# Optimization experiments

Measured on AMD Instinct MI355X. Metric: run time of the kernel, lower is better.

## Reference

```python
import jax, jax.numpy as jnp
import numpy as np

N = 100000
E = 1600000
DIMS = [64, 64, 64, 32]  # input -> hidden -> hidden -> num_classes
NEG_SLOPE = 0.01  # F.leaky_relu default


def setup_inputs() -> dict:
    key = jax.random.key(0)
    ks = jax.random.split(key, 8)
    inp = {
        "x": jax.random.normal(ks[0], (N, DIMS[0]), dtype=jnp.float32),
        "edge_index": jax.random.randint(ks[1], (2, E), 0, N, dtype=jnp.int64),
    }
    # GCNConv linear weights (glorot-ish scale) and biases
    for i in range(3):
        d_in, d_out = DIMS[i], DIMS[i + 1]
        scale = (2.0 / (d_in + d_out)) ** 0.5
        inp[f"W{i+1}"] = jax.random.normal(ks[2 + i], (d_in, d_out), dtype=jnp.float32) * scale
        inp[f"b{i+1}"] = jnp.zeros((d_out,), dtype=jnp.float32)
    return inp


def _gcn_conv(x, src, dst, norm, W, b):
    # x' = D^-1/2 (A+I) D^-1/2 (x W) + b
    h = x @ W                                   # [N, d_out]
    msg = h[src] * norm[:, None]                # gather + edge scaling  [E+N, d_out]
    out = jax.ops.segment_sum(msg, dst, num_segments=N)  # scatter-add
    return out + b


def reference(x, edge_index, W1, b1, W2, b2, W3, b3):
    loops = jnp.arange(N, dtype=edge_index.dtype)
    src = jnp.concatenate([edge_index[0], loops])  # add self-loops
    dst = jnp.concatenate([edge_index[1], loops])
    deg = jax.ops.segment_sum(jnp.ones_like(src, dtype=x.dtype), dst, num_segments=N)
    deg_isqrt = jax.lax.rsqrt(deg)              # deg >= 1 due to self-loops
    norm = deg_isqrt[src] * deg_isqrt[dst]      # [E+N]

    embeddings = []
    h = x
    for i, (W, b) in enumerate([(W1, b1), (W2, b2), (W3, b3)]):
        h = _gcn_conv(h, src, dst, norm, W, b)
        if i < 2:
            h = jnp.where(h >= 0, h, NEG_SLOPE * h)  # leaky_relu
        embeddings.append(h)
    return tuple(embeddings)
```

## Files before the change

### kernel.cpp

```cpp
#include <hip/hip_runtime.h>
#include <hip/hip_bf16.h>

typedef __hip_bfloat16 bf16;
typedef __attribute__((ext_vector_type(8))) short bf16x8;
typedef __attribute__((ext_vector_type(4))) short bf16x4;
typedef __attribute__((ext_vector_type(4))) float f32x4;

constexpr int BLK = 256;
constexpr int SCAN2_T = 512;
constexpr int NBLK = 400;

__device__ inline float s2f(short s) {
    union { unsigned u; float f; } z;
    z.u = ((unsigned)(unsigned short)s) << 16;
    return z.f;
}
__device__ inline short f2s(float f) {
    union { bf16 h; short s; } u;
    u.h = __float2bfloat16(f);
    return u.s;
}

__global__ void bucket_hist(const int* __restrict__ dst, int* __restrict__ blockhist,
                            int E, int EPB, int NB) {
    __shared__ int h[512];
    for (int i = threadIdx.x; i < NB; i += BLK) h[i] = 0;
    __syncthreads();
    int lo = blockIdx.x * EPB;
    int hi = min(E, lo + EPB);
    for (int t = lo + threadIdx.x; t < hi; t += BLK)
        atomicAdd(&h[dst[t] >> 8], 1);
    __syncthreads();
    for (int i = threadIdx.x; i < NB; i += BLK)
        blockhist[i * NBLK + blockIdx.x] = h[i];
}

__global__ void colscan_kernel(int* __restrict__ blockhist, int* __restrict__ btotal) {
    __shared__ int s[SCAN2_T];
    int b = blockIdx.x;
    int t = threadIdx.x;
    int v = (t < NBLK) ? blockhist[b * NBLK + t] : 0;
    s[t] = v;
    __syncthreads();
    for (int off = 1; off < SCAN2_T; off <<= 1) {
        int add = (t >= off) ? s[t - off] : 0;
        __syncthreads();
        s[t] += add;
        __syncthreads();
    }
    if (t < NBLK) blockhist[b * NBLK + t] = s[t] - v;
    if (t == SCAN2_T - 1) btotal[b] = s[SCAN2_T - 1];
}

__global__ void scan2_kernel(int* __restrict__ bsum, int nb) {
    __shared__ int s[SCAN2_T];
    int t = threadIdx.x;
    int v = (t < nb) ? bsum[t] : 0;
    s[t] = v;
    __syncthreads();
    for (int off = 1; off < SCAN2_T; off <<= 1) {
        int add = (t >= off) ? s[t - off] : 0;
        __syncthreads();
        s[t] += add;
        __syncthreads();
    }
    if (t < nb) bsum[t] = s[t] - v;
}

__global__ void bucket_scatter(const int* __restrict__ src, const int* __restrict__ dst,
                               const int* __restrict__ blockhist, const int* __restrict__ bbase,
                               int2* __restrict__ ssd, int E, int EPB, int NB) {
    __shared__ int h[512];
    for (int i = threadIdx.x; i < NB; i += BLK)
        h[i] = bbase[i] + blockhist[i * NBLK + blockIdx.x];
    __syncthreads();
    int lo = blockIdx.x * EPB;
    int hi = min(E, lo + EPB);
    for (int t = lo + threadIdx.x; t < hi; t += BLK) {
        int d = dst[t];
        int pos = atomicAdd(&h[d >> 8], 1);
        int2 e; e.x = src[t]; e.y = d;
        ssd[pos] = e;
    }
}

__global__ void bucket_csr(const int2* __restrict__ ssd, const int* __restrict__ bbase,
                           int* __restrict__ col, int* __restrict__ deg,
                           int* __restrict__ row_ptr, float* __restrict__ dinv,
                           int N, int E, int NB) {
    __shared__ int dloc[256];
    __shared__ int ss[256];
    __shared__ int cur[256];
    int b = blockIdx.x;
    int t = threadIdx.x;
    int lo = bbase[b];
    int hi = (b + 1 < NB) ? bbase[b + 1] : E;
    dloc[t] = 0;
    __syncthreads();
    for (int j = lo + t; j < hi; j += BLK)
        atomicAdd(&dloc[ssd[j].y & 255], 1);
    __syncthreads();
    int own = dloc[t];
    ss[t] = own;
    __syncthreads();
    for (int off = 1; off < 256; off <<= 1) {
        int add = (t >= off) ? ss[t - off] : 0;
        __syncthreads();
        ss[t] += add;
        __syncthreads();
    }
    int excl = ss[t] - own;
    cur[t] = lo + excl;
    int node = (b << 8) + t;
    if (node < N) {
        deg[node] = own;
        row_ptr[node] = lo + excl;
        dinv[node] = rsqrtf((float)own + 1.0f);
    }
    __syncthreads();
    for (int j = lo + t; j < hi; j += BLK) {
        int2 e = ssd[j];
        int p = atomicAdd(&cur[e.y & 255], 1);
        col[p] = e.x;
    }
}

__global__ void wconv_all(const float* __restrict__ W1, const float* __restrict__ W2,
                          const float* __restrict__ W3, bf16* __restrict__ WT1,
                          bf16* __restrict__ WT2, bf16* __restrict__ WT3) {
    int idx = blockIdx.x * blockDim.x + threadIdx.x;
    if (idx < 4096) {
        int k = idx >> 6, c = idx & 63;
        WT1[c * 64 + k] = __float2bfloat16(W1[idx]);
    } else if (idx < 8192) {
        int i = idx - 4096, k = i >> 6, c = i & 63;
        WT2[c * 64 + k] = __float2bfloat16(W2[i]);
    } else if (idx < 10240) {
        int i = idx - 8192, k = i >> 5, c = i & 31;
        WT3[c * 64 + k] = __float2bfloat16(W3[i]);
    }
}

template <int DOUT, bool AF32>
__global__ void mfma_gemm(const void* __restrict__ inv, const bf16* __restrict__ WT,
                          const float* __restrict__ dinv, bf16* __restrict__ hlin, int n) {
    constexpr int NT = DOUT / 16;
    const int lane = threadIdx.x & 63;
    const int wave = threadIdx.x >> 6;
    const int q = lane >> 4;
    const int l16 = lane & 15;
    const int row0 = blockIdx.x * 64 + wave * 16;

    int arow = row0 + l16;
    if (arow >= n) arow = n - 1;

    bf16x8 a0, a1;
    if (AF32) {
        const float* in = (const float*)inv;
        const float* p = in + (size_t)arow * 64 + q * 8;
        float4 f0 = *(const float4*)(p);
        float4 f1 = *(const float4*)(p + 4);
        float4 g0 = *(const float4*)(p + 32);
        float4 g1 = *(const float4*)(p + 36);
        bf16 t0[8] = {__float2bfloat16(f0.x), __float2bfloat16(f0.y), __float2bfloat16(f0.z), __float2bfloat16(f0.w),
                      __float2bfloat16(f1.x), __float2bfloat16(f1.y), __float2bfloat16(f1.z), __float2bfloat16(f1.w)};
        bf16 t1[8] = {__float2bfloat16(g0.x), __float2bfloat16(g0.y), __float2bfloat16(g0.z), __float2bfloat16(g0.w),
                      __float2bfloat16(g1.x), __float2bfloat16(g1.y), __float2bfloat16(g1.z), __float2bfloat16(g1.w)};
        __builtin_memcpy(&a0, t0, 16);
        __builtin_memcpy(&a1, t1, 16);
    } else {
        const bf16* in = (const bf16*)inv;
        a0 = *(const bf16x8*)(in + (size_t)arow * 64 + q * 8);
        a1 = *(const bf16x8*)(in + (size_t)arow * 64 + 32 + q * 8);
    }

    f32x4 acc[NT];
#pragma unroll
    for (int ct = 0; ct < NT; ++ct) {
        const bf16* wrow = WT + (size_t)(ct * 16 + l16) * 64 + q * 8;
        bf16x8 b0 = *(const bf16x8*)(wrow);
        bf16x8 b1 = *(const bf16x8*)(wrow + 32);
        f32x4 c = {0.f, 0.f, 0.f, 0.f};
        c = __builtin_amdgcn_mfma_f32_16x16x32_bf16(a0, b0, c, 0, 0, 0);
        c = __builtin_amdgcn_mfma_f32_16x16x32_bf16(a1, b1, c, 0, 0, 0);
        acc[ct] = c;
    }

    float dv[4];
#pragma unroll
    for (int r = 0; r < 4; ++r) {
        int rr = row0 + q * 4 + r;
        dv[r] = (rr < n) ? dinv[rr] : 0.0f;
    }
#pragma unroll
    for (int ct = 0; ct < NT; ++ct) {
#pragma unroll
        for (int r = 0; r < 4; ++r) {
            int rr = row0 + q * 4 + r;
            if (rr < n)
                hlin[(size_t)rr * DOUT + ct * 16 + l16] = __float2bfloat16(acc[ct][r] * dv[r]);
        }
    }
}

template <bool LEAKY>
__global__ void agg64_kernel(const int* __restrict__ row_ptr, const int* __restrict__ deg,
                             const int* __restrict__ col, const bf16* __restrict__ hlin,
                             const float* __restrict__ dinv, const float* __restrict__ b,
                             float* __restrict__ out, bf16* __restrict__ actb, int n) {
    const int wid = (blockIdx.x * blockDim.x + threadIdx.x) >> 6;
    const int lane = threadIdx.x & 63;
    const int sub = lane >> 4;
    const int g = (lane >> 3) & 1;
    const int fl = lane & 7;
    const int node = wid * 4 + sub;
    const int PAD = n;

    const bool valid = node < n;
    const int nc = valid ? node : n - 1;
    const int beg = row_ptr[nc];
    const int dg = valid ? deg[nc] : 0;
    const int end = beg + dg;

    float acc[8], acc2[8];
    {
        int c0 = (valid && g == 0) ? node : PAD;
        bf16x8 sv = *(const bf16x8*)(hlin + (size_t)c0 * 64 + (fl << 3));
#pragma unroll
        for (int k = 0; k < 8; ++k) { acc[k] = s2f(sv[k]); acc2[k] = 0.0f; }
    }

    int m = dg;
    m = max(m, __shfl_xor(m, 16));
    m = max(m, __shfl_xor(m, 32));
    const int iters = (m + 3) >> 2;

    int idx = beg + g;
    int c0 = col[idx < end ? idx : 0];
    int c1 = col[idx + 2 < end ? idx + 2 : 0];
    for (int j = 0; j < iters; ++j) {
        const int a0 = (idx < end) ? c0 : PAD;
        const int a1 = (idx + 2 < end) ? c1 : PAD;
        idx += 4;
        c0 = col[idx < end ? idx : 0];
        c1 = col[idx + 2 < end ? idx + 2 : 0];
        bf16x8 v0 = *(const bf16x8*)(hlin + (size_t)a0 * 64 + (fl << 3));
        bf16x8 v1 = *(const bf16x8*)(hlin + (size_t)a1 * 64 + (fl << 3));
#pragma unroll
        for (int k = 0; k < 8; ++k) { acc[k] += s2f(v0[k]); acc2[k] += s2f(v1[k]); }
    }

#pragma unroll
    for (int k = 0; k < 8; ++k) acc[k] += acc2[k];
#pragma unroll
    for (int k = 0; k < 8; ++k) acc[k] += __shfl_xor(acc[k], 8);

    const float dv = dinv[nc];
    const float4 bb0 = *(const float4*)(b + (fl << 3));
    const float4 bb1 = *(const float4*)(b + (fl << 3) + 4);
    float vals[8];
    vals[0] = acc[0] * dv + bb0.x;
    vals[1] = acc[1] * dv + bb0.y;
    vals[2] = acc[2] * dv + bb0.z;
    vals[3] = acc[3] * dv + bb0.w;
    vals[4] = acc[4] * dv + bb1.x;
    vals[5] = acc[5] * dv + bb1.y;
    vals[6] = acc[6] * dv + bb1.z;
    vals[7] = acc[7] * dv + bb1.w;
    if (LEAKY) {
#pragma unroll
        for (int k = 0; k < 8; ++k) vals[k] = (vals[k] >= 0.0f) ? vals[k] : 0.01f * vals[k];
    }
    if (valid && g == 0) {
        float* op = out + (size_t)node * 64 + (fl << 3);
        f32x4 o0 = {vals[0], vals[1], vals[2], vals[3]};
        f32x4 o1 = {vals[4], vals[5], vals[6], vals[7]};
        __builtin_nontemporal_store(o0, (f32x4*)op);
        __builtin_nontemporal_store(o1, (f32x4*)(op + 4));
        if (actb) {
            bf16x8 ob;
#pragma unroll
            for (int k = 0; k < 8; ++k) ob[k] = f2s(vals[k]);
            *(bf16x8*)(actb + (size_t)node * 64 + (fl << 3)) = ob;
        }
    }
}

__global__ void agg32_kernel(const int* __restrict__ row_ptr, const int* __restrict__ deg,
                             const int* __restrict__ col, const bf16* __restrict__ hlin,
                             const float* __restrict__ dinv, const float* __restrict__ b,
                             float* __restrict__ out, int n) {
    const int wid = (blockIdx.x * blockDim.x + threadIdx.x) >> 6;
    const int lane = threadIdx.x & 63;
    const int sub = lane >> 4;
    const int g = (lane >> 3) & 1;
    const int fl = lane & 7;
    const int node = wid * 4 + sub;
    const int PAD = 2 * n;

    const bool valid = node < n;
    const int nc = valid ? node : n - 1;
    const int beg = row_ptr[nc];
    const int dg = valid ? deg[nc] : 0;
    const int end = beg + dg;

    float acc[4], acc2[4];
    {
        int c0 = (valid && g == 0) ? node : PAD;
        bf16x4 sv = *(const bf16x4*)(hlin + (size_t)c0 * 32 + (fl << 2));
#pragma unroll
        for (int k = 0; k < 4; ++k) { acc[k] = s2f(sv[k]); acc2[k] = 0.0f; }
    }

    int m = dg;
    m = max(m, __shfl_xor(m, 16));
    m = max(m, __shfl_xor(m, 32));
    const int iters = (m + 3) >> 2;

    int idx = beg + g;
    int c0 = col[idx < end ? idx : 0];
    int c1 = col[idx + 2 < end ? idx + 2 : 0];
    for (int j = 0; j < iters; ++j) {
        const int a0 = (idx < end) ? c0 : PAD;
        const int a1 = (idx + 2 < end) ? c1 : PAD;
        idx += 4;
        c0 = col[idx < end ? idx : 0];
        c1 = col[idx + 2 < end ? idx + 2 : 0];
        bf16x4 v0 = *(const bf16x4*)(hlin + (size_t)a0 * 32 + (fl << 2));
        bf16x4 v1 = *(const bf16x4*)(hlin + (size_t)a1 * 32 + (fl << 2));
#pragma unroll
        for (int k = 0; k < 4; ++k) { acc[k] += s2f(v0[k]); acc2[k] += s2f(v1[k]); }
    }

#pragma unroll
    for (int k = 0; k < 4; ++k) acc[k] += acc2[k];
#pragma unroll
    for (int k = 0; k < 4; ++k) acc[k] += __shfl_xor(acc[k], 8);

    const float dv = dinv[nc];
    const float4 bb = *(const float4*)(b + (fl << 2));
    float vals[4];
    vals[0] = acc[0] * dv + bb.x;
    vals[1] = acc[1] * dv + bb.y;
    vals[2] = acc[2] * dv + bb.z;
    vals[3] = acc[3] * dv + bb.w;
    if (valid && g == 0) {
        f32x4 o = {vals[0], vals[1], vals[2], vals[3]};
        __builtin_nontemporal_store(o, (f32x4*)(out + (size_t)node * 32 + (fl << 2)));
    }
}

extern "C" void kernel_launch(void* const* d_in, const int* in_sizes, int n_in,
                              void* d_out, int out_size, void* d_ws, size_t ws_size,
                              hipStream_t stream) {
    const float* x  = (const float*)d_in[0];
    const int*   ei = (const int*)d_in[1];
    const float* W1 = (const float*)d_in[2];
    const float* b1 = (const float*)d_in[3];
    const float* W2 = (const float*)d_in[4];
    const float* b2 = (const float*)d_in[5];
    const float* W3 = (const float*)d_in[6];
    const float* b3 = (const float*)d_in[7];
    float* out = (float*)d_out;

    const int N = in_sizes[0] / 64;
    const int E = in_sizes[1] / 2;
    const int* src = ei;
    const int* dst = ei + E;

    const int NB  = (N + 255) >> 8;
    const int EPB = (E + NBLK - 1) / NBLK;

    char* w = (char*)d_ws;
    auto take = [&](size_t bytes) { char* p = w; w += (bytes + 15) & ~(size_t)15; return p; };
    int*   col       = (int*)take((size_t)E * 4);
    int2*  ssd       = (int2*)take((size_t)E * 8);
    bf16*  hlin      = (bf16*)take(((size_t)N * 64 + 64) * 2);
    bf16*  actb      = (bf16*)take((size_t)N * 64 * 2);
    bf16*  WT1       = (bf16*)take(64 * 64 * 2);
    bf16*  WT2       = (bf16*)take(64 * 64 * 2);
    bf16*  WT3       = (bf16*)take(32 * 64 * 2);
    int*   deg       = (int*)take((size_t)N * 4);
    int*   row_ptr   = (int*)take((size_t)N * 4);
    float* dinv      = (float*)take((size_t)N * 4);
    int*   blockhist = (int*)take((size_t)NB * NBLK * 4);
    int*   btotal    = (int*)take((size_t)SCAN2_T * 4);

    float* out0 = out;
    float* out1 = out + (size_t)N * 64;
    float* out2 = out + (size_t)N * 128;

    const int gemmBlocks = (N + 63) / 64;
    const int aggWaves = (N + 3) / 4;
    const int aggBlocks = (aggWaves * 64 + BLK - 1) / BLK;

    hipMemsetAsync(hlin + (size_t)N * 64, 0, 128, stream);

    bucket_hist<<<NBLK, BLK, 0, stream>>>(dst, blockhist, E, EPB, NB);
    colscan_kernel<<<NB, SCAN2_T, 0, stream>>>(blockhist, btotal);
    scan2_kernel<<<1, SCAN2_T, 0, stream>>>(btotal, NB);
    bucket_scatter<<<NBLK, BLK, 0, stream>>>(src, dst, blockhist, btotal, ssd, E, EPB, NB);
    bucket_csr<<<NB, BLK, 0, stream>>>(ssd, btotal, col, deg, row_ptr, dinv, N, E, NB);

    wconv_all<<<40, BLK, 0, stream>>>(W1, W2, W3, WT1, WT2, WT3);

    mfma_gemm<64, true><<<gemmBlocks, BLK, 0, stream>>>(x, WT1, dinv, hlin, N);
    agg64_kernel<true><<<aggBlocks, BLK, 0, stream>>>(
        row_ptr, deg, col, hlin, dinv, b1, out0, actb, N);

    mfma_gemm<64, false><<<gemmBlocks, BLK, 0, stream>>>(actb, WT2, dinv, hlin, N);
    agg64_kernel<true><<<aggBlocks, BLK, 0, stream>>>(
        row_ptr, deg, col, hlin, dinv, b2, out1, actb, N);

    mfma_gemm<32, false><<<gemmBlocks, BLK, 0, stream>>>(actb, WT3, dinv, hlin, N);
    agg32_kernel<<<aggBlocks, BLK, 0, stream>>>(
        row_ptr, deg, col, hlin, dinv, b3, out2, N);
}
```

Measured before the change: 277.1 us.

## Pack bucket edges into one int and unroll aggregation gathers to four

The intermediate bucket array now stores each edge as a single 32-bit word (source index shifted left by 8, OR'd with the low 8 bits of the destination) instead of an int2. This halves its write and read traffic in the scatter and CSR build kernels. The aggregation kernels now issue four neighbor row gathers per iteration instead of two, to keep more memory requests in flight, and add launch bounds of 256 threads with a minimum of 8 blocks per CU. The packing requires source indices below 2^23 (N is 100000), and the launch bounds may force register spilling.

```diff
diff --git a/kernel.cpp b/kernel.cpp
--- a/kernel.cpp
+++ b/kernel.cpp
@@ -69,7 +69,7 @@
 
 __global__ void bucket_scatter(const int* __restrict__ src, const int* __restrict__ dst,
                                const int* __restrict__ blockhist, const int* __restrict__ bbase,
-                               int2* __restrict__ ssd, int E, int EPB, int NB) {
+                               int* __restrict__ ssd, int E, int EPB, int NB) {
     __shared__ int h[512];
     for (int i = threadIdx.x; i < NB; i += BLK)
         h[i] = bbase[i] + blockhist[i * NBLK + blockIdx.x];
@@ -79,12 +79,11 @@
     for (int t = lo + threadIdx.x; t < hi; t += BLK) {
         int d = dst[t];
         int pos = atomicAdd(&h[d >> 8], 1);
-        int2 e; e.x = src[t]; e.y = d;
-        ssd[pos] = e;
-    }
-}
-
-__global__ void bucket_csr(const int2* __restrict__ ssd, const int* __restrict__ bbase,
+        ssd[pos] = (src[t] << 8) | (d & 255);
+    }
+}
+
+__global__ void bucket_csr(const int* __restrict__ ssd, const int* __restrict__ bbase,
                            int* __restrict__ col, int* __restrict__ deg,
                            int* __restrict__ row_ptr, float* __restrict__ dinv,
                            int N, int E, int NB) {
@@ -98,7 +97,7 @@
     dloc[t] = 0;
     __syncthreads();
     for (int j = lo + t; j < hi; j += BLK)
-        atomicAdd(&dloc[ssd[j].y & 255], 1);
+        atomicAdd(&dloc[ssd[j] & 255], 1);
     __syncthreads();
     int own = dloc[t];
     ss[t] = own;
@@ -119,9 +118,9 @@
     }
     __syncthreads();
     for (int j = lo + t; j < hi; j += BLK) {
-        int2 e = ssd[j];
-        int p = atomicAdd(&cur[e.y & 255], 1);
-        col[p] = e.x;
+        unsigned e = (unsigned)ssd[j];
+        int p = atomicAdd(&cur[e & 255], 1);
+        col[p] = (int)(e >> 8);
     }
 }
 
@@ -204,10 +203,11 @@
 }
 
 template <bool LEAKY>
-__global__ void agg64_kernel(const int* __restrict__ row_ptr, const int* __restrict__ deg,
-                             const int* __restrict__ col, const bf16* __restrict__ hlin,
-                             const float* __restrict__ dinv, const float* __restrict__ b,
-                             float* __restrict__ out, bf16* __restrict__ actb, int n) {
+__global__ __launch_bounds__(256, 8)
+void agg64_kernel(const int* __restrict__ row_ptr, const int* __restrict__ deg,
+                  const int* __restrict__ col, const bf16* __restrict__ hlin,
+                  const float* __restrict__ dinv, const float* __restrict__ b,
+                  float* __restrict__ out, bf16* __restrict__ actb, int n) {
     const int wid = (blockIdx.x * blockDim.x + threadIdx.x) >> 6;
     const int lane = threadIdx.x & 63;
     const int sub = lane >> 4;
@@ -233,21 +233,32 @@
     int m = dg;
     m = max(m, __shfl_xor(m, 16));
     m = max(m, __shfl_xor(m, 32));
-    const int iters = (m + 3) >> 2;
+    const int iters = (m + 7) >> 3;
 
     int idx = beg + g;
-    int c0 = col[idx < end ? idx : 0];
+    int c0 = col[idx     < end ? idx     : 0];
     int c1 = col[idx + 2 < end ? idx + 2 : 0];
+    int c2 = col[idx + 4 < end ? idx + 4 : 0];
+    int c3 = col[idx + 6 < end ? idx + 6 : 0];
     for (int j = 0; j < iters; ++j) {
-        const int a0 = (idx < end) ? c0 : PAD;
+        const int a0 = (idx     < end) ? c0 : PAD;
         const int a1 = (idx + 2 < end) ? c1 : PAD;
-        idx += 4;
-        c0 = col[idx < end ? idx : 0];
+        const int a2 = (idx + 4 < end) ? c2 : PAD;
+        const int a3 = (idx + 6 < end) ? c3 : PAD;
+        idx += 8;
+        c0 = col[idx     < end ? idx     : 0];
         c1 = col[idx + 2 < end ? idx + 2 : 0];
+        c2 = col[idx + 4 < end ? idx + 4 : 0];
+        c3 = col[idx + 6 < end ? idx + 6 : 0];
         bf16x8 v0 = *(const bf16x8*)(hlin + (size_t)a0 * 64 + (fl << 3));
         bf16x8 v1 = *(const bf16x8*)(hlin + (size_t)a1 * 64 + (fl << 3));
-#pragma unroll
-        for (int k = 0; k < 8; ++k) { acc[k] += s2f(v0[k]); acc2[k] += s2f(v1[k]); }
+        bf16x8 v2 = *(const bf16x8*)(hlin + (size_t)a2 * 64 + (fl << 3));
+        bf16x8 v3 = *(const bf16x8*)(hlin + (size_t)a3 * 64 + (fl << 3));
+#pragma unroll
+        for (int k = 0; k < 8; ++k) {
+            acc[k]  += s2f(v0[k]) + s2f(v1[k]);
+            acc2[k] += s2f(v2[k]) + s2f(v3[k]);
+        }
     }
 
 #pragma unroll
@@ -286,10 +297,11 @@
     }
 }
 
-__global__ void agg32_kernel(const int* __restrict__ row_ptr, const int* __restrict__ deg,
-                             const int* __restrict__ col, const bf16* __restrict__ hlin,
-                             const float* __restrict__ dinv, const float* __restrict__ b,
-                             float* __restrict__ out, int n) {
+__global__ __launch_bounds__(256, 8)
+void agg32_kernel(const int* __restrict__ row_ptr, const int* __restrict__ deg,
+                  const int* __restrict__ col, const bf16* __restrict__ hlin,
+                  const float* __restrict__ dinv, const float* __restrict__ b,
+                  float* __restrict__ out, int n) {
     const int wid = (blockIdx.x * blockDim.x + threadIdx.x) >> 6;
     const int lane = threadIdx.x & 63;
     const int sub = lane >> 4;
@@ -315,21 +327,32 @@
     int m = dg;
     m = max(m, __shfl_xor(m, 16));
     m = max(m, __shfl_xor(m, 32));
-    const int iters = (m + 3) >> 2;
+    const int iters = (m + 7) >> 3;
 
     int idx = beg + g;
-    int c0 = col[idx < end ? idx : 0];
+    int c0 = col[idx     < end ? idx     : 0];
     int c1 = col[idx + 2 < end ? idx + 2 : 0];
+    int c2 = col[idx + 4 < end ? idx + 4 : 0];
+    int c3 = col[idx + 6 < end ? idx + 6 : 0];
     for (int j = 0; j < iters; ++j) {
-        const int a0 = (idx < end) ? c0 : PAD;
+        const int a0 = (idx     < end) ? c0 : PAD;
         const int a1 = (idx + 2 < end) ? c1 : PAD;
-        idx += 4;
-        c0 = col[idx < end ? idx : 0];
+        const int a2 = (idx + 4 < end) ? c2 : PAD;
+        const int a3 = (idx + 6 < end) ? c3 : PAD;
+        idx += 8;
+        c0 = col[idx     < end ? idx     : 0];
         c1 = col[idx + 2 < end ? idx + 2 : 0];
+        c2 = col[idx + 4 < end ? idx + 4 : 0];
+        c3 = col[idx + 6 < end ? idx + 6 : 0];
         bf16x4 v0 = *(const bf16x4*)(hlin + (size_t)a0 * 32 + (fl << 2));
         bf16x4 v1 = *(const bf16x4*)(hlin + (size_t)a1 * 32 + (fl << 2));
-#pragma unroll
-        for (int k = 0; k < 4; ++k) { acc[k] += s2f(v0[k]); acc2[k] += s2f(v1[k]); }
+        bf16x4 v2 = *(const bf16x4*)(hlin + (size_t)a2 * 32 + (fl << 2));
+        bf16x4 v3 = *(const bf16x4*)(hlin + (size_t)a3 * 32 + (fl << 2));
+#pragma unroll
+        for (int k = 0; k < 4; ++k) {
+            acc[k]  += s2f(v0[k]) + s2f(v1[k]);
+            acc2[k] += s2f(v2[k]) + s2f(v3[k]);
+        }
     }
 
 #pragma unroll
@@ -374,7 +397,7 @@
     char* w = (char*)d_ws;
     auto take = [&](size_t bytes) { char* p = w; w += (bytes + 15) & ~(size_t)15; return p; };
     int*   col       = (int*)take((size_t)E * 4);
-    int2*  ssd       = (int2*)take((size_t)E * 8);
+    int*   ssd       = (int*)take((size_t)E * 4);
     bf16*  hlin      = (bf16*)take(((size_t)N * 64 + 64) * 2);
     bf16*  actb      = (bf16*)take((size_t)N * 64 * 2);
     bf16*  WT1       = (bf16*)take(64 * 64 * 2);
```

Result: faster. 269.8 us (-2.6%).
